# Kernel tuning notes

Measured on AMD Instinct MI355X. Metric: run time of the kernel, lower is better.

## Reference

```python
import jax, jax.numpy as jnp
import numpy as np


def setup_inputs() -> dict:
    key = jax.random.key(0)
    k1, k2 = jax.random.split(key)
    N, M, D = 8192, 8192, 512
    x = jax.random.normal(k1, (N, D), dtype=jnp.float32)
    y = jax.random.normal(k2, (M, D), dtype=jnp.float32)
    gamma = jnp.float32(1.0)
    return {"x": x, "y": y, "gamma": gamma}


def reference(x, y, gamma):
    # k(x, y) = exp(-gamma * ||x - y||^2)
    x = x.reshape(-1, x.shape[-1])
    y = y.reshape(-1, y.shape[-1])
    x_sq = jnp.sum(x * x, axis=-1)  # [N]
    y_sq = jnp.sum(y * y, axis=-1)  # [M]
    cross = x @ y.T                  # [N, M]
    sq_dist = x_sq[:, None] + y_sq[None, :] - 2.0 * cross
    sq_dist = jnp.maximum(sq_dist, 0.0)  # guard tiny negative roundoff
    return jnp.exp(-gamma * sq_dist)
```

## Files before the change

kernel.cpp:

```cpp
#include <hip/hip_runtime.h>
#include <hip/hip_bf16.h>

typedef unsigned short u16;
typedef __attribute__((ext_vector_type(8))) short bf16x8;
typedef __attribute__((ext_vector_type(4))) float f32x4;

typedef const __attribute__((address_space(1))) void gvoid_t;
typedef __attribute__((address_space(3))) void lvoid_t;

__device__ __forceinline__ void gload_lds16(const void* g, void* l) {
  __builtin_amdgcn_global_load_lds((gvoid_t*)g, (lvoid_t*)l, 16, 0, 0);
}

__device__ __forceinline__ u16 f2bf(float f) {
  union { float f; unsigned u; } a;
  a.f = f;
  unsigned r = (a.u + 0x7FFFu + ((a.u >> 16) & 1u)) >> 16;
  return (u16)r;
}

__global__ __launch_bounds__(128) void rbf_prep(
    const float* __restrict__ x, const float* __restrict__ y,
    u16* __restrict__ xb, u16* __restrict__ yb,
    float* __restrict__ xsq, float* __restrict__ ysq,
    int N, int M, int D) {
  int row = blockIdx.x;
  const float* src;
  u16* dst;
  float* sq;
  if (row < N) {
    src = x + (size_t)row * D;
    dst = xb + (size_t)row * D;
    sq = xsq + row;
  } else {
    int r = row - N;
    src = y + (size_t)r * D;
    dst = yb + (size_t)r * D;
    sq = ysq + r;
  }
  int t = threadIdx.x;
  float4 v = reinterpret_cast<const float4*>(src)[t];
  float s = v.x * v.x + v.y * v.y + v.z * v.z + v.w * v.w;
  ushort4 o;
  o.x = f2bf(v.x);
  o.y = f2bf(v.y);
  o.z = f2bf(v.z);
  o.w = f2bf(v.w);
  reinterpret_cast<ushort4*>(dst)[t] = o;
  #pragma unroll
  for (int off = 32; off > 0; off >>= 1) s += __shfl_down(s, off, 64);
  __shared__ float red[2];
  if ((t & 63) == 0) red[t >> 6] = s;
  __syncthreads();
  if (t == 0) sq[0] = red[0] + red[1];
}

#define BM 256
#define BN 256
#define BK 64

__global__ __launch_bounds__(512, 2) void rbf_gemm(
    const u16* __restrict__ xb, const u16* __restrict__ yb,
    const float* __restrict__ xsq, const float* __restrict__ ysq,
    const float* __restrict__ gptr, float* __restrict__ out,
    int N, int M, int D) {
  __shared__ u16 lds[2][2][BM * BK];

  int bid = blockIdx.x;
  int nbr = N / BM, nbc = M / BN;
  int trow, tcol;
  if (nbr == 32 && nbc == 32) {
    int xcd = bid & 7;
    int s = bid >> 3;
    trow = ((xcd >> 1) << 3) + (s & 7);
    tcol = ((xcd & 1) << 4) + (s >> 3);
  } else {
    int cpx = gridDim.x >> 3;
    int swz = (bid & 7) * cpx + (bid >> 3);
    trow = swz / nbc;
    tcol = swz % nbc;
  }
  int brow = trow * BM;
  int bcol = tcol * BN;

  int tid = threadIdx.x;
  int w = tid >> 6;
  int lane = tid & 63;
  int wm = w >> 2;
  int wn = w & 3;
  int fr = lane & 15;
  int fq = lane >> 4;

  int srow = lane >> 3;
  int scol = ((lane & 7) ^ (srow & 7)) * 8;
  const u16* xsrc = xb + (size_t)(brow + w * 32 + srow) * D + scol;
  const u16* ysrc = yb + (size_t)(bcol + w * 32 + srow) * D + scol;
  int sdst = w * 2048;

  int cxor = (fr & 7) * 8;
  int colx0 = (fq * 8) ^ cxor;
  int colx1 = (32 + fq * 8) ^ cxor;
  int aoff0 = (wm * 128 + fr) * 64 + colx0;
  int aoff1 = (wm * 128 + fr) * 64 + colx1;
  int boff0 = (wn * 64 + fr) * 64 + colx0;
  int boff1 = (wn * 64 + fr) * 64 + colx1;

  f32x4 acc[8][4];
  #pragma unroll
  for (int m = 0; m < 8; ++m)
    #pragma unroll
    for (int n = 0; n < 4; ++n)
      acc[m][n] = (f32x4){0.f, 0.f, 0.f, 0.f};

  auto stage = [&](int kt, int b) {
    const u16* xs = xsrc + kt * 64;
    const u16* ys = ysrc + kt * 64;
    u16* la = &lds[b][0][sdst];
    u16* lb = &lds[b][1][sdst];
    #pragma unroll
    for (int i = 0; i < 4; ++i)
      gload_lds16(xs + (size_t)i * 8 * D, la + i * 512);
    #pragma unroll
    for (int i = 0; i < 4; ++i)
      gload_lds16(ys + (size_t)i * 8 * D, lb + i * 512);
  };

#define PHASE(MH, NH, RA, RB)                                                  \
  {                                                                            \
    if (RA) {                                                                  \
      _Pragma("unroll") for (int mi = 0; mi < 4; ++mi) {                       \
        af[mi][0] = *(const bf16x8*)&A[aoff0 + (MH * 4 + mi) * 1024];          \
        af[mi][1] = *(const bf16x8*)&A[aoff1 + (MH * 4 + mi) * 1024];          \
      }                                                                        \
    }                                                                          \
    if (RB) {                                                                  \
      _Pragma("unroll") for (int ni = 0; ni < 2; ++ni) {                       \
        bf[ni][0] = *(const bf16x8*)&B[boff0 + (NH * 2 + ni) * 1024];          \
        bf[ni][1] = *(const bf16x8*)&B[boff1 + (NH * 2 + ni) * 1024];          \
      }                                                                        \
    }                                                                          \
    __builtin_amdgcn_s_setprio(1);                                             \
    _Pragma("unroll") for (int mi = 0; mi < 4; ++mi)                           \
      _Pragma("unroll") for (int ni = 0; ni < 2; ++ni) {                       \
        acc[MH * 4 + mi][NH * 2 + ni] =                                        \
            __builtin_amdgcn_mfma_f32_16x16x32_bf16(                           \
                bf[ni][0], af[mi][0], acc[MH * 4 + mi][NH * 2 + ni], 0, 0, 0); \
        acc[MH * 4 + mi][NH * 2 + ni] =                                        \
            __builtin_amdgcn_mfma_f32_16x16x32_bf16(                           \
                bf[ni][1], af[mi][1], acc[MH * 4 + mi][NH * 2 + ni], 0, 0, 0); \
      }                                                                        \
    __builtin_amdgcn_s_setprio(0);                                             \
  }

  int nkt = D >> 6;
  stage(0, 0);
  stage(1, 1);
  for (int t = 0; t < nkt; ++t) {
    int b = t & 1;
    if (t + 1 < nkt)
      asm volatile("s_waitcnt vmcnt(8)" ::: "memory");
    else
      asm volatile("s_waitcnt vmcnt(0)" ::: "memory");
    __builtin_amdgcn_sched_barrier(0);
    __builtin_amdgcn_s_barrier();
    __builtin_amdgcn_sched_barrier(0);

    const u16* A = &lds[b][0][0];
    const u16* B = &lds[b][1][0];
    bf16x8 af[4][2], bf[2][2];

    PHASE(0, 0, true, true);
    __builtin_amdgcn_s_barrier();
    PHASE(0, 1, false, true);
    __builtin_amdgcn_s_barrier();
    PHASE(1, 1, true, false);
    __builtin_amdgcn_s_barrier();
    PHASE(1, 0, false, true);

    asm volatile("s_waitcnt lgkmcnt(0)" ::: "memory");
    __builtin_amdgcn_sched_barrier(0);
    __builtin_amdgcn_s_barrier();
    __builtin_amdgcn_sched_barrier(0);
    if (t + 2 < nkt) stage(t + 2, b);
  }
#undef PHASE

  float gamma = gptr[0];
  #pragma unroll
  for (int m = 0; m < 8; ++m) {
    int i = brow + wm * 128 + m * 16 + fr;
    float xs = xsq[i];
    size_t ro = (size_t)i * M;
    #pragma unroll
    for (int n = 0; n < 4; ++n) {
      int jb = bcol + wn * 64 + n * 16 + fq * 4;
      float4 ys4 = *reinterpret_cast<const float4*>(&ysq[jb]);
      float4 e;
      e.x = __expf(-gamma * fmaxf(xs + ys4.x - 2.0f * acc[m][n][0], 0.0f));
      e.y = __expf(-gamma * fmaxf(xs + ys4.y - 2.0f * acc[m][n][1], 0.0f));
      e.z = __expf(-gamma * fmaxf(xs + ys4.z - 2.0f * acc[m][n][2], 0.0f));
      e.w = __expf(-gamma * fmaxf(xs + ys4.w - 2.0f * acc[m][n][3], 0.0f));
      *reinterpret_cast<float4*>(&out[ro + jb]) = e;
    }
  }
}

__global__ __launch_bounds__(256) void rbf_naive(
    const float* __restrict__ x, const float* __restrict__ y,
    const float* __restrict__ gptr, float* __restrict__ out,
    int N, int M, int D) {
  __shared__ float xs[16][17];
  __shared__ float ys[16][17];
  int nbn = M / 16;
  int brow = (blockIdx.x / nbn) * 16;
  int bcol = (blockIdx.x % nbn) * 16;
  int ti = threadIdx.x >> 4, tj = threadIdx.x & 15;
  float dacc = 0.f, xacc = 0.f, yacc = 0.f;
  for (int k0 = 0; k0 < D; k0 += 16) {
    xs[ti][tj] = x[(size_t)(brow + ti) * D + k0 + tj];
    ys[ti][tj] = y[(size_t)(bcol + ti) * D + k0 + tj];
    __syncthreads();
    #pragma unroll
    for (int kk = 0; kk < 16; ++kk) {
      float xv = xs[ti][kk], yv = ys[tj][kk];
      dacc += xv * yv;
      xacc += xv * xv;
      yacc += yv * yv;
    }
    __syncthreads();
  }
  float gamma = gptr[0];
  float d2 = fmaxf(xacc + yacc - 2.f * dacc, 0.f);
  out[(size_t)(brow + ti) * M + (bcol + tj)] = __expf(-gamma * d2);
}

extern "C" void kernel_launch(void* const* d_in, const int* in_sizes, int n_in,
                              void* d_out, int out_size, void* d_ws,
                              size_t ws_size, hipStream_t stream) {
  const float* x = (const float*)d_in[0];
  const float* y = (const float*)d_in[1];
  const float* g = (const float*)d_in[2];
  float* out = (float*)d_out;

  const int D = 512;
  const int N = in_sizes[0] / D;
  const int M = in_sizes[1] / D;

  size_t need = (size_t)(N + M) * D * sizeof(u16) + (size_t)(N + M) * sizeof(float);
  bool shapes_ok = (N % BM == 0) && (M % BN == 0) && (D % BK == 0) && (D / BK >= 2);

  if (ws_size >= need && shapes_ok) {
    u16* xb = (u16*)d_ws;
    u16* yb = xb + (size_t)N * D;
    float* xsq = (float*)(yb + (size_t)M * D);
    float* ysq = xsq + N;

    rbf_prep<<<N + M, 128, 0, stream>>>(x, y, xb, yb, xsq, ysq, N, M, D);
    int nwg = (N / BM) * (M / BN);
    rbf_gemm<<<nwg, 512, 0, stream>>>(xb, yb, xsq, ysq, g, out, N, M, D);
  } else {
    rbf_naive<<<(N / 16) * (M / 16), 256, 0, stream>>>(x, y, g, out, N, M, D);
  }
}
```

Baseline: 132.3 us.

## Shrink GEMM tiles to 128x128 with 256 threads and simplify inner loop

Cuts the workgroup tile from 256x256 to 128x128 with 4 waves instead of 8. This gives 4096 workgroups, reworks the XCD-aware tile swizzle for the 64x64 grid, and replaces the four-phase barrier-interleaved MFMA schedule with a single load-then-compute block per k-step. The epilogue is rewritten to fold gamma and the log2(e) scaling into an FMA followed by exp2f, with the y-norm terms precomputed once per thread. Smaller tiles aim for better occupancy and load balance, but reduce operand reuse per LDS byte and raise global re-reads of x and y.

```diff
diff --git a/kernel.cpp b/kernel.cpp
--- a/kernel.cpp
+++ b/kernel.cpp
@@ -55,11 +55,11 @@
   if (t == 0) sq[0] = red[0] + red[1];
 }
 
-#define BM 256
-#define BN 256
+#define BM 128
+#define BN 128
 #define BK 64
 
-__global__ __launch_bounds__(512, 2) void rbf_gemm(
+__global__ __launch_bounds__(256, 2) void rbf_gemm(
     const u16* __restrict__ xb, const u16* __restrict__ yb,
     const float* __restrict__ xsq, const float* __restrict__ ysq,
     const float* __restrict__ gptr, float* __restrict__ out,
@@ -69,11 +69,13 @@
   int bid = blockIdx.x;
   int nbr = N / BM, nbc = M / BN;
   int trow, tcol;
-  if (nbr == 32 && nbc == 32) {
+  if (nbr == 64 && nbc == 64) {
     int xcd = bid & 7;
     int s = bid >> 3;
-    trow = ((xcd >> 1) << 3) + (s & 7);
-    tcol = ((xcd & 1) << 4) + (s >> 3);
+    int gr = s >> 6;
+    int q = s & 63;
+    trow = gr * 8 + (q & 7);
+    tcol = xcd * 8 + (q >> 3);
   } else {
     int cpx = gridDim.x >> 3;
     int swz = (bid & 7) * cpx + (bid >> 3);
@@ -86,13 +88,13 @@
   int tid = threadIdx.x;
   int w = tid >> 6;
   int lane = tid & 63;
-  int wm = w >> 2;
-  int wn = w & 3;
+  int wm = w >> 1;
+  int wn = w & 1;
   int fr = lane & 15;
   int fq = lane >> 4;
 
   int srow = lane >> 3;
-  int scol = ((lane & 7) ^ (srow & 7)) * 8;
+  int scol = ((lane & 7) ^ srow) * 8;
   const u16* xsrc = xb + (size_t)(brow + w * 32 + srow) * D + scol;
   const u16* ysrc = yb + (size_t)(bcol + w * 32 + srow) * D + scol;
   int sdst = w * 2048;
@@ -100,14 +102,12 @@
   int cxor = (fr & 7) * 8;
   int colx0 = (fq * 8) ^ cxor;
   int colx1 = (32 + fq * 8) ^ cxor;
-  int aoff0 = (wm * 128 + fr) * 64 + colx0;
-  int aoff1 = (wm * 128 + fr) * 64 + colx1;
-  int boff0 = (wn * 64 + fr) * 64 + colx0;
-  int boff1 = (wn * 64 + fr) * 64 + colx1;
-
-  f32x4 acc[8][4];
-  #pragma unroll
-  for (int m = 0; m < 8; ++m)
+  int arow0 = (wm * 64 + fr) * 64;
+  int brow0 = (wn * 64 + fr) * 64;
+
+  f32x4 acc[4][4];
+  #pragma unroll
+  for (int m = 0; m < 4; ++m)
     #pragma unroll
     for (int n = 0; n < 4; ++n)
       acc[m][n] = (f32x4){0.f, 0.f, 0.f, 0.f};
@@ -124,33 +124,6 @@
     for (int i = 0; i < 4; ++i)
       gload_lds16(ys + (size_t)i * 8 * D, lb + i * 512);
   };
-
-#define PHASE(MH, NH, RA, RB)                                                  \
-  {                                                                            \
-    if (RA) {                                                                  \
-      _Pragma("unroll") for (int mi = 0; mi < 4; ++mi) {                       \
-        af[mi][0] = *(const bf16x8*)&A[aoff0 + (MH * 4 + mi) * 1024];          \
-        af[mi][1] = *(const bf16x8*)&A[aoff1 + (MH * 4 + mi) * 1024];          \
-      }                                                                        \
-    }                                                                          \
-    if (RB) {                                                                  \
-      _Pragma("unroll") for (int ni = 0; ni < 2; ++ni) {                       \
-        bf[ni][0] = *(const bf16x8*)&B[boff0 + (NH * 2 + ni) * 1024];          \
-        bf[ni][1] = *(const bf16x8*)&B[boff1 + (NH * 2 + ni) * 1024];          \
-      }                                                                        \
-    }                                                                          \
-    __builtin_amdgcn_s_setprio(1);                                             \
-    _Pragma("unroll") for (int mi = 0; mi < 4; ++mi)                           \
-      _Pragma("unroll") for (int ni = 0; ni < 2; ++ni) {                       \
-        acc[MH * 4 + mi][NH * 2 + ni] =                                        \
-            __builtin_amdgcn_mfma_f32_16x16x32_bf16(                           \
-                bf[ni][0], af[mi][0], acc[MH * 4 + mi][NH * 2 + ni], 0, 0, 0); \
-        acc[MH * 4 + mi][NH * 2 + ni] =                                        \
-            __builtin_amdgcn_mfma_f32_16x16x32_bf16(                           \
-                bf[ni][1], af[mi][1], acc[MH * 4 + mi][NH * 2 + ni], 0, 0, 0); \
-      }                                                                        \
-    __builtin_amdgcn_s_setprio(0);                                             \
-  }
 
   int nkt = D >> 6;
   stage(0, 0);
@@ -167,39 +140,62 @@
 
     const u16* A = &lds[b][0][0];
     const u16* B = &lds[b][1][0];
-    bf16x8 af[4][2], bf[2][2];
-
-    PHASE(0, 0, true, true);
+    bf16x8 af[4][2], bf[4][2];
+    #pragma unroll
+    for (int m = 0; m < 4; ++m) {
+      af[m][0] = *(const bf16x8*)&A[arow0 + m * 1024 + colx0];
+      af[m][1] = *(const bf16x8*)&A[arow0 + m * 1024 + colx1];
+    }
+    #pragma unroll
+    for (int n = 0; n < 4; ++n) {
+      bf[n][0] = *(const bf16x8*)&B[brow0 + n * 1024 + colx0];
+      bf[n][1] = *(const bf16x8*)&B[brow0 + n * 1024 + colx1];
+    }
+
+    __builtin_amdgcn_s_setprio(1);
+    #pragma unroll
+    for (int m = 0; m < 4; ++m)
+      #pragma unroll
+      for (int n = 0; n < 4; ++n) {
+        acc[m][n] = __builtin_amdgcn_mfma_f32_16x16x32_bf16(
+            bf[n][0], af[m][0], acc[m][n], 0, 0, 0);
+        acc[m][n] = __builtin_amdgcn_mfma_f32_16x16x32_bf16(
+            bf[n][1], af[m][1], acc[m][n], 0, 0, 0);
+      }
+    __builtin_amdgcn_s_setprio(0);
+
+    asm volatile("s_waitcnt lgkmcnt(0)" ::: "memory");
+    __builtin_amdgcn_sched_barrier(0);
     __builtin_amdgcn_s_barrier();
-    PHASE(0, 1, false, true);
-    __builtin_amdgcn_s_barrier();
-    PHASE(1, 1, true, false);
-    __builtin_amdgcn_s_barrier();
-    PHASE(1, 0, false, true);
-
-    asm volatile("s_waitcnt lgkmcnt(0)" ::: "memory");
-    __builtin_amdgcn_sched_barrier(0);
-    __builtin_amdgcn_s_barrier();
     __builtin_amdgcn_sched_barrier(0);
     if (t + 2 < nkt) stage(t + 2, b);
   }
-#undef PHASE
-
-  float gamma = gptr[0];
-  #pragma unroll
-  for (int m = 0; m < 8; ++m) {
-    int i = brow + wm * 128 + m * 16 + fr;
-    float xs = xsq[i];
+
+  float gl2 = gptr[0] * 1.44269504088896f;
+  float m2gl2 = 2.0f * gl2;
+  float4 gys[4];
+  #pragma unroll
+  for (int n = 0; n < 4; ++n) {
+    float4 t4 = *reinterpret_cast<const float4*>(
+        &ysq[bcol + wn * 64 + n * 16 + fq * 4]);
+    gys[n].x = gl2 * t4.x;
+    gys[n].y = gl2 * t4.y;
+    gys[n].z = gl2 * t4.z;
+    gys[n].w = gl2 * t4.w;
+  }
+  #pragma unroll
+  for (int m = 0; m < 4; ++m) {
+    int i = brow + wm * 64 + m * 16 + fr;
+    float gxs = gl2 * xsq[i];
     size_t ro = (size_t)i * M;
     #pragma unroll
     for (int n = 0; n < 4; ++n) {
       int jb = bcol + wn * 64 + n * 16 + fq * 4;
-      float4 ys4 = *reinterpret_cast<const float4*>(&ysq[jb]);
       float4 e;
-      e.x = __expf(-gamma * fmaxf(xs + ys4.x - 2.0f * acc[m][n][0], 0.0f));
-      e.y = __expf(-gamma * fmaxf(xs + ys4.y - 2.0f * acc[m][n][1], 0.0f));
-      e.z = __expf(-gamma * fmaxf(xs + ys4.z - 2.0f * acc[m][n][2], 0.0f));
-      e.w = __expf(-gamma * fmaxf(xs + ys4.w - 2.0f * acc[m][n][3], 0.0f));
+      e.x = exp2f(fminf(fmaf(m2gl2, acc[m][n][0], -(gxs + gys[n].x)), 0.f));
+      e.y = exp2f(fminf(fmaf(m2gl2, acc[m][n][1], -(gxs + gys[n].y)), 0.f));
+      e.z = exp2f(fminf(fmaf(m2gl2, acc[m][n][2], -(gxs + gys[n].z)), 0.f));
+      e.w = exp2f(fminf(fmaf(m2gl2, acc[m][n][3], -(gxs + gys[n].w)), 0.f));
       *reinterpret_cast<float4*>(&out[ro + jb]) = e;
     }
   }
@@ -257,7 +253,7 @@
 
     rbf_prep<<<N + M, 128, 0, stream>>>(x, y, xb, yb, xsq, ysq, N, M, D);
     int nwg = (N / BM) * (M / BN);
-    rbf_gemm<<<nwg, 512, 0, stream>>>(xb, yb, xsq, ysq, g, out, N, M, D);
+    rbf_gemm<<<nwg, 256, 0, stream>>>(xb, yb, xsq, ysq, g, out, N, M, D);
   } else {
     rbf_naive<<<(N / 16) * (M / 16), 256, 0, stream>>>(x, y, g, out, N, M, D);
   }
```

After: 112.7 us. 14.8% less time.
